# Performance work log

Measured on AMD Instinct MI355X. Metric: run time of the kernel, lower is better.

Reference implementation:

```python
import jax, jax.numpy as jnp
import numpy as np

B, S, D, H = 2, 2048, 2048, 32
DH = D // H
NEG = -1e9


def setup_inputs() -> dict:
    key = jax.random.key(0)
    ks = jax.random.split(key, 10)
    sc = 0.02
    hidden_state = jax.random.normal(ks[0], (B, S, D), dtype=jnp.float32)
    # additive causal mask, broadcastable to [B,H,S,S]
    causal = jnp.tril(jnp.ones((S, S), dtype=bool))
    mask = jnp.where(causal, 0.0, NEG).astype(jnp.float32)[None, None]
    return {
        "hidden_state": hidden_state,
        "mask": mask,
        "q_w": jax.random.normal(ks[1], (D, D), jnp.float32) * sc,
        "q_b": jnp.zeros((D,), jnp.float32),
        "k_w": jax.random.normal(ks[2], (D, D), jnp.float32) * sc,
        "k_b": jnp.zeros((D,), jnp.float32),
        "v_w": jax.random.normal(ks[3], (D, D), jnp.float32) * sc,
        "v_b": jnp.zeros((D,), jnp.float32),
        "o_w": jax.random.normal(ks[4], (D, D), jnp.float32) * sc,
        "o_b": jnp.zeros((D,), jnp.float32),
    }


def reference(hidden_state, mask, q_w, q_b, k_w, k_b, v_w, v_b, o_w, o_b):
    scale = DH ** -0.5
    # projections (torch Linear: x @ W^T + b)
    q = (hidden_state @ q_w.T + q_b).reshape(B, S, H, DH).transpose(0, 2, 1, 3) * scale
    k = (hidden_state @ k_w.T + k_b).reshape(B, S, H, DH).transpose(0, 2, 1, 3)
    v = (hidden_state @ v_w.T + v_b).reshape(B, S, H, DH).transpose(0, 2, 1, 3)
    qk = jnp.einsum('bhqd,bhkd->bhqk', q, k) + mask
    attn = jax.nn.softmax(qk, axis=-1)
    o = jnp.einsum('bhqk,bhkd->bhqd', attn, v)
    o = o.transpose(0, 2, 1, 3).reshape(B, S, D)
    return o @ o_w.T + o_b
```

## Files before the change

### kernel.cpp

```cpp
#include <hip/hip_runtime.h>
#include <stdint.h>

#define Hh   32
#define Ss   2048
#define Dd   2048
#define DHd  64
#define Mtok 4096
#define MiB  (1u << 20)
#define NTK  32

typedef unsigned short u16;
typedef u16   u16x4  __attribute__((ext_vector_type(4)));
typedef u16   u16x8  __attribute__((ext_vector_type(8)));
typedef short bf16x8 __attribute__((ext_vector_type(8)));
typedef float f32x4  __attribute__((ext_vector_type(4)));

__device__ __forceinline__ u16 f2bf(float f) {
    union { float f; uint32_t u; } v; v.f = f;
    uint32_t r = v.u + 0x7fffu + ((v.u >> 16) & 1u);
    return (u16)(r >> 16);
}
__device__ __forceinline__ uint32_t cvtpk_bf16(float lo, float hi) {
    uint32_t r;
    asm volatile("v_cvt_pk_bf16_f32 %0, %1, %2" : "=v"(r) : "v"(lo), "v"(hi));
    return r;
}
__device__ __forceinline__ void gld_lds16(const void* g, void* l) {
    __builtin_amdgcn_global_load_lds(
        (const __attribute__((address_space(1))) uint32_t*)g,
        (__attribute__((address_space(3))) uint32_t*)l,
        16, 0, 0);
}
#define SB() __builtin_amdgcn_sched_barrier(0)

__global__ void cvt_bf16(const float* __restrict__ src, u16* __restrict__ dst, int n)
{
    const int i = (blockIdx.x * 256 + threadIdx.x) * 8;
    if (i + 8 > n) return;
    f32x4 a = *(const f32x4*)(src + i);
    f32x4 b = *(const f32x4*)(src + i + 4);
    u16x8 o;
    o[0] = f2bf(a[0]); o[1] = f2bf(a[1]); o[2] = f2bf(a[2]); o[3] = f2bf(a[3]);
    o[4] = f2bf(b[0]); o[5] = f2bf(b[1]); o[6] = f2bf(b[2]); o[7] = f2bf(b[3]);
    *(u16x8*)(dst + i) = o;
}


__device__ __forceinline__ void stage_unitA(const u16* __restrict__ src, u16* dst, int wid, int lane)
{
    const int P = wid * 64 + lane;
    const int rp = P >> 3, c4p = P & 7, c4 = c4p ^ (rp & 7);
    const int r = rp * 2 + (c4 >> 2), c = (c4 & 3) * 8;
    gld_lds16(src + (size_t)r * Dd + c, dst + wid * 512);
}
__device__ __forceinline__ void stage_unitB(const u16* __restrict__ src, u16* dst, int wid, int lane)
{
#pragma unroll
    for (int j = 0; j < 2; ++j) {
        const int P = j * 512 + wid * 64 + lane;
        const int rp = P >> 3, c4p = P & 7, c4 = c4p ^ (rp & 7);
        const int r = rp * 2 + (c4 >> 2), c = (c4 & 3) * 8;
        gld_lds16(src + (size_t)r * Dd + c, dst + j * 4096 + wid * 512);
    }
}
__device__ __forceinline__ bf16x8 frag_read(const u16* unit, int r, int lg)
{
    const int rp = r >> 1;
    const int c4 = ((r & 1) << 2) | lg;
    const int c4p = c4 ^ (rp & 7);
    return *(const bf16x8*)(unit + rp * 64 + c4p * 8);
}

__device__ __forceinline__ void gemm8_core(const u16* __restrict__ Ab, const u16* __restrict__ Wb,
                                           u16* L, f32x4 acc[4][4],
                                           int wid, int lane, int l15, int lg, int wm, int wn)
{
    u16* const L0 = L;
    u16* const L1 = L + 24576;
    stage_unitB(Wb + 0,  L0 + 8192,  wid, lane);
    stage_unitA(Ab + 0,  L0 + 0,     wid, lane);
    stage_unitB(Wb + 32, L0 + 16384, wid, lane);
    stage_unitA(Ab + 32, L0 + 4096,  wid, lane);
    stage_unitB(Wb + 64, L1 + 8192,  wid, lane);
    stage_unitA(Ab + 64, L1 + 0,     wid, lane);
    stage_unitB(Wb + 96, L1 + 16384, wid, lane);
    asm volatile("s_waitcnt vmcnt(5)" ::: "memory");
    SB(); __builtin_amdgcn_s_barrier(); SB();

    bf16x8 bfr[4];
    const int aro = wm * 64 + l15;
    const int bro = wn * 64 + l15;
#pragma unroll 2
    for (int t = 0; t < NTK; ++t) {
        u16* const Lc = (t & 1) ? L1 : L0;
        u16* const Ln = (t & 1) ? L0 : L1;
#pragma unroll
        for (int ph = 0; ph < 4; ++ph) {
            const int ks = ph >> 1, hf = ph & 1;
            const u16* Au = Lc + ks * 4096;
            const u16* Bu = Lc + 8192 + ks * 8192;
            if (hf == 0) {
#pragma unroll
                for (int ni = 0; ni < 4; ++ni)
                    bfr[ni] = frag_read(Bu, bro + ni * 16, lg);
            }
            bf16x8 a0 = frag_read(Au, aro + (hf * 2 + 0) * 16, lg);
            bf16x8 a1 = frag_read(Au, aro + (hf * 2 + 1) * 16, lg);
            if      (ph == 0) { if (t + 1 < NTK) stage_unitA(Ab + (t + 1) * 64 + 32, Ln + 4096,  wid, lane); }
            else if (ph == 1) { if (t + 2 < NTK) stage_unitB(Wb + (t + 2) * 64 + 0,  Lc + 8192,  wid, lane); }
            else if (ph == 2) { if (t + 2 < NTK) stage_unitA(Ab + (t + 2) * 64 + 0,  Lc + 0,     wid, lane); }
            else              { if (t + 2 < NTK) stage_unitB(Wb + (t + 2) * 64 + 32, Lc + 16384, wid, lane); }
            SB(); __builtin_amdgcn_s_barrier(); SB();
            asm volatile("s_waitcnt lgkmcnt(0)" ::: "memory");
            SB();
            __builtin_amdgcn_s_setprio(1);
#pragma unroll
            for (int ni = 0; ni < 4; ++ni) {
                acc[hf * 2 + 0][ni] = __builtin_amdgcn_mfma_f32_16x16x32_bf16(a0, bfr[ni], acc[hf * 2 + 0][ni], 0, 0, 0);
                acc[hf * 2 + 1][ni] = __builtin_amdgcn_mfma_f32_16x16x32_bf16(a1, bfr[ni], acc[hf * 2 + 1][ni], 0, 0, 0);
            }
            __builtin_amdgcn_s_setprio(0);
            if (ph == 3 && t < NTK - 1) {
                if (t + 2 < NTK) { asm volatile("s_waitcnt vmcnt(5)" ::: "memory"); }
                else             { asm volatile("s_waitcnt vmcnt(0)" ::: "memory"); }
            }
            SB(); __builtin_amdgcn_s_barrier(); SB();
        }
    }
}

__global__ __launch_bounds__(512) void gemm_qkv8(
    const u16* __restrict__ X, const u16* __restrict__ Wcat,
    const float* __restrict__ Bq, const float* __restrict__ Bk, const float* __restrict__ Bv,
    u16* __restrict__ Qo, u16* __restrict__ Ko, u16* __restrict__ Vo)
{
    __shared__ __align__(16) u16 L[2 * 24576];
    const int tid = threadIdx.x, wid = tid >> 6, lane = tid & 63;
    const int l15 = lane & 15, lg = lane >> 4;
    const int wm = wid >> 2, wn = wid & 3;
    const int m0 = blockIdx.x * 128, n0 = blockIdx.y * 256;

    f32x4 acc[4][4] = {};
    gemm8_core(X + (size_t)m0 * Dd, Wcat + (size_t)n0 * Dd, L, acc, wid, lane, l15, lg, wm, wn);

#pragma unroll
    for (int ni = 0; ni < 4; ++ni) {
        const int n = n0 + wn * 64 + ni * 16 + l15;
        const int z = n >> 11, nn = n & 2047;
        const float bv = (z == 0 ? Bq : z == 1 ? Bk : Bv)[nn];
        const float sc = (z == 0) ? 0.125f : 1.0f;
        u16* Out = (z == 0 ? Qo : z == 1 ? Ko : Vo);
        const int h = nn >> 6, dh = nn & 63;
#pragma unroll
        for (int mi = 0; mi < 4; ++mi)
#pragma unroll
            for (int r = 0; r < 4; ++r) {
                const int m = m0 + wm * 64 + mi * 16 + lg * 4 + r;
                const int b = m >> 11, s = m & 2047;
                Out[(((size_t)b * Hh + h) * Ss + s) * DHd + dh] = f2bf((acc[mi][ni][r] + bv) * sc);
            }
    }
}

__global__ __launch_bounds__(512) void gemm_oproj8(
    const u16* __restrict__ A, const u16* __restrict__ W,
    const float* __restrict__ Bi, float* __restrict__ Out)
{
    __shared__ __align__(16) u16 L[2 * 24576];
    const int tid = threadIdx.x, wid = tid >> 6, lane = tid & 63;
    const int l15 = lane & 15, lg = lane >> 4;
    const int wm = wid >> 2, wn = wid & 3;
    const int m0 = blockIdx.x * 128, n0 = blockIdx.y * 256;

    f32x4 acc[4][4] = {};
    gemm8_core(A + (size_t)m0 * Dd, W + (size_t)n0 * Dd, L, acc, wid, lane, l15, lg, wm, wn);

#pragma unroll
    for (int ni = 0; ni < 4; ++ni) {
        const int n = n0 + wn * 64 + ni * 16 + l15;
        const float bv = Bi[n];
#pragma unroll
        for (int mi = 0; mi < 4; ++mi)
#pragma unroll
            for (int r = 0; r < 4; ++r) {
                const int m = m0 + wm * 64 + mi * 16 + lg * 4 + r;
                Out[(size_t)m * Dd + n] = acc[mi][ni][r] + bv;
            }
    }
}

__global__ void transpose_v(const u16* __restrict__ Vsrc, u16* __restrict__ Vdst)
{
    __shared__ __align__(16) u16 t[64 * 68];
    const int bh = blockIdx.y, s0 = blockIdx.x * 64;
    const int tid = threadIdx.x;
    {
        const int r = tid >> 2, cq = (tid & 3) * 16;
        const u16* src = Vsrc + ((size_t)bh * Ss + s0 + r) * DHd;
#pragma unroll
        for (int j = 0; j < 4; ++j) {
            u16x4 v = *(const u16x4*)(src + cq + j * 4);
            *(u16x4*)&t[r * 68 + cq + j * 4] = v;
        }
    }
    __syncthreads();
    {
        const int d = tid >> 2, sq = (tid & 3) * 16;
        u16* dst = Vdst + ((size_t)bh * DHd + d) * Ss + s0;
#pragma unroll
        for (int j = 0; j < 4; ++j) {
            u16x4 v;
            v.x = t[(sq + j * 4 + 0) * 68 + d];
            v.y = t[(sq + j * 4 + 1) * 68 + d];
            v.z = t[(sq + j * 4 + 2) * 68 + d];
            v.w = t[(sq + j * 4 + 3) * 68 + d];
            *(u16x4*)(dst + sq + j * 4) = v;
        }
    }
}

__device__ __forceinline__ void stage_kv(const u16* __restrict__ Kg, const u16* __restrict__ Vg,
                                         u16* Kl, u16* Vl, int kv0, int tid)
{
    const int u    = tid;
    const int row  = u >> 3;
    const int csrc = ((u & 7) ^ (row & 7)) * 8;
    const int base = (u & ~63) * 8;
    gld_lds16(Kg + (size_t)(kv0 + row) * DHd + csrc, Kl + base);
    gld_lds16(Vg + (size_t)row * Ss + kv0 + csrc, Vl + base);
}

__device__ __forceinline__ void attn_tile(
    const u16* __restrict__ Kc, const u16* __restrict__ Vc, int kv0,
    int q0, int qrow, int l15, int lg, int psw,
    const bf16x8* __restrict__ bq, f32x4* __restrict__ o,
    float& m_r, float& l_r, char* __restrict__ prow)
{
    if (kv0 > q0 + 15) return;
    f32x4 s[4] = {};
    __builtin_amdgcn_s_setprio(1);
#pragma unroll
    for (int nb = 0; nb < 4; ++nb) {
        const int krow = nb * 16 + l15;
        const char* rb = (const char*)(Kc + krow * 64);
        const int sw = (krow & 7) << 4;
#pragma unroll
        for (int kf = 0; kf < 2; ++kf) {
            bf16x8 ak = *(const bf16x8*)(rb + ((kf * 64 + lg * 16) ^ sw));
            s[nb] = __builtin_amdgcn_mfma_f32_16x16x32_bf16(ak, bq[kf], s[nb], 0, 0, 0);
        }
    }
    __builtin_amdgcn_s_setprio(0);
    if (kv0 + 63 > q0) {
#pragma unroll
        for (int nb = 0; nb < 4; ++nb)
#pragma unroll
            for (int r = 0; r < 4; ++r)
                if (kv0 + nb * 16 + lg * 4 + r > qrow) s[nb][r] = -3e38f;
    }
    float pm = -3e38f;
#pragma unroll
    for (int nb = 0; nb < 4; ++nb)
#pragma unroll
        for (int r = 0; r < 4; ++r) pm = fmaxf(pm, s[nb][r]);
    pm = fmaxf(pm, __shfl_xor(pm, 16, 64));
    pm = fmaxf(pm, __shfl_xor(pm, 32, 64));
    const bool full = !__all(pm - m_r <= 8.0f);
    float mn = m_r, al = 1.0f;
    if (full) {
        mn = fmaxf(m_r, pm);
        al = __expf(m_r - mn);
#pragma unroll
        for (int nb = 0; nb < 4; ++nb)
#pragma unroll
            for (int r = 0; r < 4; ++r) o[nb][r] *= al;
    }
    float rs = 0.f;
    float p[4][4];
#pragma unroll
    for (int nb = 0; nb < 4; ++nb)
#pragma unroll
        for (int r = 0; r < 4; ++r) { p[nb][r] = __expf(s[nb][r] - mn); rs += p[nb][r]; }
    rs += __shfl_xor(rs, 16, 64);
    rs += __shfl_xor(rs, 32, 64);
    l_r = l_r * al + rs;
    m_r = mn;
#pragma unroll
    for (int nb = 0; nb < 4; ++nb) {
        const uint32_t w0 = cvtpk_bf16(p[nb][0], p[nb][1]);
        const uint32_t w1 = cvtpk_bf16(p[nb][2], p[nb][3]);
        const int c0 = (nb * 32 + lg * 8) ^ psw;
        *(uint32_t*)(prow + c0)     = w0;
        *(uint32_t*)(prow + c0 + 4) = w1;
    }
    bf16x8 pa[2];
#pragma unroll
    for (int ks = 0; ks < 2; ++ks)
        pa[ks] = *(const bf16x8*)(prow + ((ks * 64 + lg * 16) ^ psw));
    __builtin_amdgcn_s_setprio(1);
#pragma unroll
    for (int nb = 0; nb < 4; ++nb) {
        const int vrow = nb * 16 + l15;
        const char* rb = (const char*)(Vc + vrow * 64);
        const int sw = (vrow & 7) << 4;
#pragma unroll
        for (int ks = 0; ks < 2; ++ks) {
            bf16x8 bv = *(const bf16x8*)(rb + ((ks * 64 + lg * 16) ^ sw));
            o[nb] = __builtin_amdgcn_mfma_f32_16x16x32_bf16(bv, pa[ks], o[nb], 0, 0, 0);
        }
    }
    __builtin_amdgcn_s_setprio(0);
}

__global__ __launch_bounds__(512) void attn(
    const u16* __restrict__ Qb, const u16* __restrict__ Kb,
    const u16* __restrict__ Vt, u16* __restrict__ Ob)
{
    __shared__ __align__(16) u16 Kl[2][4096];
    __shared__ __align__(16) u16 Vl[2][4096];
    __shared__ __align__(16) u16 PlA[8][1024];
    __shared__ __align__(16) u16 PlB[8][1024];
    const int bh = blockIdx.y;
    const int b = bh >> 5, h = bh & 31;
    const int tid = threadIdx.x;
    const int wid = tid >> 6, lane = tid & 63;
    const int l15 = lane & 15, lg = lane >> 4;
    const int bxA = blockIdx.x, bxB = 15 - bxA;
    const int q0A = bxA * 128 + wid * 16, q0B = bxB * 128 + wid * 16;
    const int qrowA = q0A + l15, qrowB = q0B + l15;
    char* prowA = (char*)PlA[wid] + l15 * 128;
    char* prowB = (char*)PlB[wid] + l15 * 128;
    const int psw = (l15 & 7) << 4;

    const u16* Kp = Kb + (size_t)bh * Ss * DHd;
    const u16* Vp = Vt + (size_t)bh * DHd * Ss;

    bf16x8 bqA[2], bqB[2];
    {
        const u16* QpA = Qb + ((size_t)bh * Ss + q0A) * DHd;
        const u16* QpB = Qb + ((size_t)bh * Ss + q0B) * DHd;
#pragma unroll
        for (int kf = 0; kf < 2; ++kf) {
            bqA[kf] = *(const bf16x8*)(QpA + (size_t)l15 * DHd + kf * 32 + lg * 8);
            bqB[kf] = *(const bf16x8*)(QpB + (size_t)l15 * DHd + kf * 32 + lg * 8);
        }
    }
    asm volatile("s_waitcnt vmcnt(0)" ::: "memory");

    f32x4 oA[4] = {}, oB[4] = {};
    float mA = -3e38f, lA = 0.f, mB = -3e38f, lB = 0.f;
    const int nt = 2 * (bxB + 1);

    stage_kv(Kp, Vp, Kl[0], Vl[0], 0, tid);
    for (int t = 0; t < nt; ++t) {
        if (t + 1 < nt) {
            stage_kv(Kp, Vp, Kl[(t + 1) & 1], Vl[(t + 1) & 1], (t + 1) * 64, tid);
            asm volatile("s_waitcnt vmcnt(2)" ::: "memory");
        } else {
            asm volatile("s_waitcnt vmcnt(0)" ::: "memory");
        }
        SB(); __builtin_amdgcn_s_barrier(); SB();
        const int kv0 = t * 64;
        attn_tile(Kl[t & 1], Vl[t & 1], kv0, q0A, qrowA, l15, lg, psw, bqA, oA, mA, lA, prowA);
        attn_tile(Kl[t & 1], Vl[t & 1], kv0, q0B, qrowB, l15, lg, psw, bqB, oB, mB, lB, prowB);
        SB(); __builtin_amdgcn_s_barrier(); SB();
    }

    {
        const float inv = 1.0f / lA;
        u16* orow = Ob + ((size_t)b * Ss + qrowA) * Dd + h * DHd;
#pragma unroll
        for (int nb = 0; nb < 4; ++nb) {
            u16x4 pk;
#pragma unroll
            for (int r = 0; r < 4; ++r) pk[r] = f2bf(oA[nb][r] * inv);
            *(u16x4*)(orow + nb * 16 + lg * 4) = pk;
        }
    }
    {
        const float inv = 1.0f / lB;
        u16* orow = Ob + ((size_t)b * Ss + qrowB) * Dd + h * DHd;
#pragma unroll
        for (int nb = 0; nb < 4; ++nb) {
            u16x4 pk;
#pragma unroll
            for (int r = 0; r < 4; ++r) pk[r] = f2bf(oB[nb][r] * inv);
            *(u16x4*)(orow + nb * 16 + lg * 4) = pk;
        }
    }
}

extern "C" void kernel_launch(void* const* d_in, const int* in_sizes, int n_in,
                              void* d_out, int out_size, void* d_ws, size_t ws_size,
                              hipStream_t stream)
{
    (void)in_sizes; (void)n_in; (void)out_size; (void)ws_size;
    const float* x  = (const float*)d_in[0];
    const float* qw = (const float*)d_in[2];
    const float* qb = (const float*)d_in[3];
    const float* kw = (const float*)d_in[4];
    const float* kb = (const float*)d_in[5];
    const float* vw = (const float*)d_in[6];
    const float* vb = (const float*)d_in[7];
    const float* ow = (const float*)d_in[8];
    const float* obias = (const float*)d_in[9];

    uint8_t* ws = (uint8_t*)d_ws;
    u16* Xb  = (u16*)(ws);
    u16* Wcat= (u16*)(ws + 16 * MiB);
    u16* Wob = (u16*)(ws + 40 * MiB);
    u16* Qb  = (u16*)(ws + 48 * MiB);
    u16* Kb  = (u16*)(ws + 64 * MiB);
    u16* Vb  = (u16*)(ws + 80 * MiB);
    u16* Vt  = Xb;
    u16* Ob  = Vb;

    const int nX = Mtok * Dd;
    const int nW = Dd * Dd;
    dim3 blk(256);
    cvt_bf16<<<nX / 2048, blk, 0, stream>>>(x,  Xb,  nX);
    cvt_bf16<<<nW / 2048, blk, 0, stream>>>(qw, Wcat,          nW);
    cvt_bf16<<<nW / 2048, blk, 0, stream>>>(kw, Wcat + nW,     nW);
    cvt_bf16<<<nW / 2048, blk, 0, stream>>>(vw, Wcat + 2 * nW, nW);
    cvt_bf16<<<nW / 2048, blk, 0, stream>>>(ow, Wob, nW);

    gemm_qkv8<<<dim3(Mtok / 128, 6144 / 256), dim3(512), 0, stream>>>(
        Xb, Wcat, qb, kb, vb, Qb, Kb, Vb);
    transpose_v<<<dim3(Ss / 64, 64), blk, 0, stream>>>(Vb, Vt);
    attn<<<dim3(8, 64), dim3(512), 0, stream>>>(Qb, Kb, Vt, Ob);
    gemm_oproj8<<<dim3(Mtok / 128, Dd / 256), dim3(512), 0, stream>>>(
        Ob, Wob, obias, (float*)d_out);
}
```

Before: 248.3 us.

## Halve GEMM barrier phases per k-tile and fuse bf16 conversion launches

The shared GEMM core now runs two phases per 64-wide k-tile instead of four. Each phase loads all four A and four B fragments, issues 16 MFMAs, and stages a full A+B half-unit pair, which removes one of the two barriers per phase and halves the phase count. The prefetch schedule and vmcnt waits are reworked to match. The five separate fp32-to-bf16 conversion launches are merged into one kernel that picks source and destination by index range, cutting launch overhead. The GEMM change raises register pressure and puts more global loads in flight per phase.

```diff
diff --git a/kernel.cpp b/kernel.cpp
--- a/kernel.cpp
+++ b/kernel.cpp
@@ -33,16 +33,28 @@
 }
 #define SB() __builtin_amdgcn_sched_barrier(0)
 
-__global__ void cvt_bf16(const float* __restrict__ src, u16* __restrict__ dst, int n)
-{
-    const int i = (blockIdx.x * 256 + threadIdx.x) * 8;
-    if (i + 8 > n) return;
-    f32x4 a = *(const f32x4*)(src + i);
-    f32x4 b = *(const f32x4*)(src + i + 4);
+__global__ void cvt_all(const float* __restrict__ x,  const float* __restrict__ qw,
+                        const float* __restrict__ kw, const float* __restrict__ vw,
+                        const float* __restrict__ ow,
+                        u16* __restrict__ Xb, u16* __restrict__ Wcat, u16* __restrict__ Wob)
+{
+    const size_t nX = 1u << 23, nW = 1u << 22;
+    size_t i = ((size_t)blockIdx.x * 256 + threadIdx.x) * 8;
+    const float* src; u16* dst; size_t off;
+    if (i < nX) { src = x; dst = Xb; off = i; }
+    else {
+        size_t j = i - nX;
+        int seg = (int)(j >> 22);
+        off = j & (nW - 1);
+        src = (seg == 0) ? qw : (seg == 1) ? kw : (seg == 2) ? vw : ow;
+        dst = (seg == 3) ? Wob : Wcat + (size_t)seg * nW;
+    }
+    f32x4 a = *(const f32x4*)(src + off);
+    f32x4 b = *(const f32x4*)(src + off + 4);
     u16x8 o;
     o[0] = f2bf(a[0]); o[1] = f2bf(a[1]); o[2] = f2bf(a[2]); o[3] = f2bf(a[3]);
     o[4] = f2bf(b[0]); o[5] = f2bf(b[1]); o[6] = f2bf(b[2]); o[7] = f2bf(b[3]);
-    *(u16x8*)(dst + i) = o;
+    *(u16x8*)(dst + off) = o;
 }
 
 
@@ -71,23 +83,21 @@
     return *(const bf16x8*)(unit + rp * 64 + c4p * 8);
 }
 
-__device__ __forceinline__ void gemm8_core(const u16* __restrict__ Ab, const u16* __restrict__ Wb,
+__device__ __forceinline__ void gemm2_core(const u16* __restrict__ Ab, const u16* __restrict__ Wb,
                                            u16* L, f32x4 acc[4][4],
                                            int wid, int lane, int l15, int lg, int wm, int wn)
 {
     u16* const L0 = L;
     u16* const L1 = L + 24576;
+    stage_unitA(Ab + 0,  L0 + 0,     wid, lane);
     stage_unitB(Wb + 0,  L0 + 8192,  wid, lane);
-    stage_unitA(Ab + 0,  L0 + 0,     wid, lane);
+    stage_unitA(Ab + 32, L0 + 4096,  wid, lane);
     stage_unitB(Wb + 32, L0 + 16384, wid, lane);
-    stage_unitA(Ab + 32, L0 + 4096,  wid, lane);
+    stage_unitA(Ab + 64, L1 + 0,     wid, lane);
     stage_unitB(Wb + 64, L1 + 8192,  wid, lane);
-    stage_unitA(Ab + 64, L1 + 0,     wid, lane);
-    stage_unitB(Wb + 96, L1 + 16384, wid, lane);
-    asm volatile("s_waitcnt vmcnt(5)" ::: "memory");
+    asm volatile("s_waitcnt vmcnt(6)" ::: "memory");
     SB(); __builtin_amdgcn_s_barrier(); SB();
 
-    bf16x8 bfr[4];
     const int aro = wm * 64 + l15;
     const int bro = wn * 64 + l15;
 #pragma unroll 2
@@ -95,35 +105,37 @@
         u16* const Lc = (t & 1) ? L1 : L0;
         u16* const Ln = (t & 1) ? L0 : L1;
 #pragma unroll
-        for (int ph = 0; ph < 4; ++ph) {
-            const int ks = ph >> 1, hf = ph & 1;
-            const u16* Au = Lc + ks * 4096;
-            const u16* Bu = Lc + 8192 + ks * 8192;
-            if (hf == 0) {
-#pragma unroll
-                for (int ni = 0; ni < 4; ++ni)
-                    bfr[ni] = frag_read(Bu, bro + ni * 16, lg);
+        for (int ph = 0; ph < 2; ++ph) {
+            const u16* Au = Lc + ph * 4096;
+            const u16* Bu = Lc + 8192 + ph * 8192;
+            bf16x8 bfr[4], a[4];
+#pragma unroll
+            for (int ni = 0; ni < 4; ++ni) bfr[ni] = frag_read(Bu, bro + ni * 16, lg);
+#pragma unroll
+            for (int mi = 0; mi < 4; ++mi) a[mi] = frag_read(Au, aro + mi * 16, lg);
+            if (ph == 0) {
+                if (t + 1 < NTK) {
+                    stage_unitA(Ab + (t + 1) * 64 + 32, Ln + 4096,  wid, lane);
+                    stage_unitB(Wb + (t + 1) * 64 + 32, Ln + 16384, wid, lane);
+                }
+            } else {
+                if (t + 2 < NTK) {
+                    stage_unitA(Ab + (t + 2) * 64, Lc + 0,    wid, lane);
+                    stage_unitB(Wb + (t + 2) * 64, Lc + 8192, wid, lane);
+                }
             }
-            bf16x8 a0 = frag_read(Au, aro + (hf * 2 + 0) * 16, lg);
-            bf16x8 a1 = frag_read(Au, aro + (hf * 2 + 1) * 16, lg);
-            if      (ph == 0) { if (t + 1 < NTK) stage_unitA(Ab + (t + 1) * 64 + 32, Ln + 4096,  wid, lane); }
-            else if (ph == 1) { if (t + 2 < NTK) stage_unitB(Wb + (t + 2) * 64 + 0,  Lc + 8192,  wid, lane); }
-            else if (ph == 2) { if (t + 2 < NTK) stage_unitA(Ab + (t + 2) * 64 + 0,  Lc + 0,     wid, lane); }
-            else              { if (t + 2 < NTK) stage_unitB(Wb + (t + 2) * 64 + 32, Lc + 16384, wid, lane); }
-            SB(); __builtin_amdgcn_s_barrier(); SB();
             asm volatile("s_waitcnt lgkmcnt(0)" ::: "memory");
             SB();
             __builtin_amdgcn_s_setprio(1);
 #pragma unroll
-            for (int ni = 0; ni < 4; ++ni) {
-                acc[hf * 2 + 0][ni] = __builtin_amdgcn_mfma_f32_16x16x32_bf16(a0, bfr[ni], acc[hf * 2 + 0][ni], 0, 0, 0);
-                acc[hf * 2 + 1][ni] = __builtin_amdgcn_mfma_f32_16x16x32_bf16(a1, bfr[ni], acc[hf * 2 + 1][ni], 0, 0, 0);
-            }
+            for (int mi = 0; mi < 4; ++mi)
+#pragma unroll
+                for (int ni = 0; ni < 4; ++ni)
+                    acc[mi][ni] = __builtin_amdgcn_mfma_f32_16x16x32_bf16(a[mi], bfr[ni], acc[mi][ni], 0, 0, 0);
             __builtin_amdgcn_s_setprio(0);
-            if (ph == 3 && t < NTK - 1) {
-                if (t + 2 < NTK) { asm volatile("s_waitcnt vmcnt(5)" ::: "memory"); }
-                else             { asm volatile("s_waitcnt vmcnt(0)" ::: "memory"); }
-            }
+            const bool deep = (ph == 0) ? (t + 1 < NTK) : (t + 2 < NTK);
+            if (deep) { asm volatile("s_waitcnt vmcnt(6)" ::: "memory"); }
+            else      { asm volatile("s_waitcnt vmcnt(0)" ::: "memory"); }
             SB(); __builtin_amdgcn_s_barrier(); SB();
         }
     }
@@ -141,7 +153,7 @@
     const int m0 = blockIdx.x * 128, n0 = blockIdx.y * 256;
 
     f32x4 acc[4][4] = {};
-    gemm8_core(X + (size_t)m0 * Dd, Wcat + (size_t)n0 * Dd, L, acc, wid, lane, l15, lg, wm, wn);
+    gemm2_core(X + (size_t)m0 * Dd, Wcat + (size_t)n0 * Dd, L, acc, wid, lane, l15, lg, wm, wn);
 
 #pragma unroll
     for (int ni = 0; ni < 4; ++ni) {
@@ -173,7 +185,7 @@
     const int m0 = blockIdx.x * 128, n0 = blockIdx.y * 256;
 
     f32x4 acc[4][4] = {};
-    gemm8_core(A + (size_t)m0 * Dd, W + (size_t)n0 * Dd, L, acc, wid, lane, l15, lg, wm, wn);
+    gemm2_core(A + (size_t)m0 * Dd, W + (size_t)n0 * Dd, L, acc, wid, lane, l15, lg, wm, wn);
 
 #pragma unroll
     for (int ni = 0; ni < 4; ++ni) {
@@ -415,18 +427,11 @@
     u16* Vt  = Xb;
     u16* Ob  = Vb;
 
-    const int nX = Mtok * Dd;
-    const int nW = Dd * Dd;
-    dim3 blk(256);
-    cvt_bf16<<<nX / 2048, blk, 0, stream>>>(x,  Xb,  nX);
-    cvt_bf16<<<nW / 2048, blk, 0, stream>>>(qw, Wcat,          nW);
-    cvt_bf16<<<nW / 2048, blk, 0, stream>>>(kw, Wcat + nW,     nW);
-    cvt_bf16<<<nW / 2048, blk, 0, stream>>>(vw, Wcat + 2 * nW, nW);
-    cvt_bf16<<<nW / 2048, blk, 0, stream>>>(ow, Wob, nW);
+    cvt_all<<<12288, 256, 0, stream>>>(x, qw, kw, vw, ow, Xb, Wcat, Wob);
 
     gemm_qkv8<<<dim3(Mtok / 128, 6144 / 256), dim3(512), 0, stream>>>(
         Xb, Wcat, qb, kb, vb, Qb, Kb, Vb);
-    transpose_v<<<dim3(Ss / 64, 64), blk, 0, stream>>>(Vb, Vt);
+    transpose_v<<<dim3(Ss / 64, 64), dim3(256), 0, stream>>>(Vb, Vt);
     attn<<<dim3(8, 64), dim3(512), 0, stream>>>(Qb, Kb, Vt, Ob);
     gemm_oproj8<<<dim3(Mtok / 128, Dd / 256), dim3(512), 0, stream>>>(
         Ob, Wob, obias, (float*)d_out);
```

Result: faster. 239.2 us (-3.7%).
